# Performance work log

Hardware: AMD Instinct MI355X
Metric: run time of the kernel (lower is better)

Reference implementation:

```python
import jax, jax.numpy as jnp
import numpy as np
from jax import lax

B = 65536

def _conv(x, w, b):
    y = lax.conv_general_dilated(x, w, (1, 1), 'VALID',
                                 dimension_numbers=('NCHW', 'OIHW', 'NCHW'))
    return y + b[None, :, None, None]

def _maxpool2(x):
    return lax.reduce_window(x, -jnp.inf, lax.max, (1, 1, 2, 2), (1, 1, 2, 2), 'VALID')

def _cnot01(s):  # control wire0, target wire1; s: [B,2,2] indexed [b,q0,q1]
    return jnp.stack([s[:, 0, :], s[:, 1, ::-1]], axis=1)

def _cnot10(s):  # control wire1, target wire0
    return jnp.stack([s[:, :, 0], s[:, ::-1, 1]], axis=2)

def _ry(half_angle):  # RY(2*half_angle) as used in circuit (theta/2 = half_angle)
    c, si = jnp.cos(half_angle), jnp.sin(half_angle)
    return jnp.stack([jnp.stack([c, -si]), jnp.stack([si, c])]).astype(jnp.complex64)

def _apply_w0(s, U):
    return jnp.einsum('ij,bjk->bik', U, s)

def _apply_w1(s, U):
    return jnp.einsum('ij,bkj->bki', U, s)

def _quantum(x2, p):
    # x2: [B,2] float32, p: [8] float32. Batched 2-qubit statevector sim.
    x0, x1 = x2[:, 0], x2[:, 1]
    n = x2.shape[0]
    s = jnp.full((n, 2, 2), 0.5 + 0.0j, dtype=jnp.complex64)  # H|0> x H|0>
    # RZ(2*x0) on wire 0: diag(e^{-i x0}, e^{i x0})
    s = s * jnp.exp(1j * jnp.stack([-x0, x0], axis=1).astype(jnp.complex64))[:, :, None]
    # RZ(2*x1) on wire 1
    s = s * jnp.exp(1j * jnp.stack([-x1, x1], axis=1).astype(jnp.complex64))[:, None, :]
    s = _cnot01(s)
    ang = (jnp.pi - x0) * (jnp.pi - x1)  # RZ(2*ang) on wire 1
    s = s * jnp.exp(1j * jnp.stack([-ang, ang], axis=1).astype(jnp.complex64))[:, None, :]
    s = _cnot01(s)
    s = _apply_w0(s, _ry(p[0])); s = _apply_w1(s, _ry(p[1])); s = _cnot01(s)
    s = _apply_w0(s, _ry(p[2])); s = _apply_w1(s, _ry(p[3])); s = _cnot10(s)
    s = _apply_w0(s, _ry(p[4])); s = _apply_w1(s, _ry(p[5])); s = _cnot01(s)
    s = _apply_w0(s, _ry(p[6])); s = _apply_w1(s, _ry(p[7]))
    z = jnp.array([[1.0, -1.0], [-1.0, 1.0]], dtype=jnp.float32)  # Z0 (x) Z1 signs
    prob = (s.real ** 2 + s.imag ** 2)
    return jnp.sum(prob * z[None], axis=(1, 2))  # [B]

def setup_inputs() -> dict:
    key = jax.random.key(0)
    ks = jax.random.split(key, 12)
    d = {}
    d['x'] = jax.random.normal(ks[0], (B, 1, 28, 28), dtype=jnp.float32)
    d['conv1_w'] = jax.random.normal(ks[1], (2, 1, 5, 5), dtype=jnp.float32) * 0.2
    d['conv1_b'] = jax.random.normal(ks[2], (2,), dtype=jnp.float32) * 0.1
    d['conv2_w'] = jax.random.normal(ks[3], (16, 2, 5, 5), dtype=jnp.float32) * 0.14
    d['conv2_b'] = jax.random.normal(ks[4], (16,), dtype=jnp.float32) * 0.1
    d['fc1_w'] = jax.random.normal(ks[5], (64, 256), dtype=jnp.float32) * 0.0625
    d['fc1_b'] = jax.random.normal(ks[6], (64,), dtype=jnp.float32) * 0.05
    d['fc2_w'] = jax.random.normal(ks[7], (2, 64), dtype=jnp.float32) * 0.125
    d['fc2_b'] = jax.random.normal(ks[8], (2,), dtype=jnp.float32) * 0.05
    d['fc3_w'] = jax.random.normal(ks[9], (1, 1), dtype=jnp.float32)
    d['fc3_b'] = jax.random.normal(ks[10], (1,), dtype=jnp.float32) * 0.05
    d['qnn_params'] = jax.random.uniform(ks[11], (8,), dtype=jnp.float32)
    return d

def reference(x, conv1_w, conv1_b, conv2_w, conv2_b, fc1_w, fc1_b,
              fc2_w, fc2_b, fc3_w, fc3_b, qnn_params):
    h = jax.nn.relu(_conv(x, conv1_w, conv1_b))        # [B,2,24,24]
    h = _maxpool2(h)                                    # [B,2,12,12]
    h = jax.nn.relu(_conv(h, conv2_w, conv2_b))        # [B,16,8,8]
    h = _maxpool2(h)                                    # [B,16,4,4]
    # Dropout2d: identity in eval mode
    h = h.reshape(h.shape[0], -1)                       # [B,256]
    h = jax.nn.relu(h @ fc1_w.T + fc1_b)                # [B,64]
    h = h @ fc2_w.T + fc2_b                             # [B,2]
    q = _quantum(h, qnn_params)[:, None]                # [B,1]
    y = q @ fc3_w.T + fc3_b                             # [B,1]
    logits = jnp.concatenate([y, 1.0 - y], axis=-1)     # [B,2]
    return jax.nn.log_softmax(logits, axis=1)
```

## Files before the change

### kernel.cpp

```cpp
#include <hip/hip_runtime.h>
#include <math.h>


typedef float v2f __attribute__((ext_vector_type(2)));
typedef float f32x4 __attribute__((ext_vector_type(4)));
typedef short bf16x8 __attribute__((ext_vector_type(8)));

union B8 { unsigned int u[4]; bf16x8 v; };

static __device__ __forceinline__ v2f vfma2(v2f a, float w, v2f c) {
    return __builtin_elementwise_fma(a, (v2f){w, w}, c);
}
static __device__ __forceinline__ v2f vmax2(v2f a, v2f b) {
    return __builtin_elementwise_max(a, b);
}

#define PK_FMA_W0(acc, w, xp) \
    asm("v_pk_fma_f32 %0, %1, %2, %0 op_sel:[0,0,0] op_sel_hi:[1,0,1]" \
        : "+v"(acc) : "s"(w), "v"(xp))
#define PK_FMA_W1(acc, w, xp) \
    asm("v_pk_fma_f32 %0, %1, %2, %0 op_sel:[0,1,0] op_sel_hi:[1,1,1]" \
        : "+v"(acc) : "s"(w), "v"(xp))

#define MFMA16(a, b, c) __builtin_amdgcn_mfma_f32_16x16x32_bf16(a, b, c, 0, 0, 0)

static __device__ __forceinline__ void pack_hilo(const float* f, bf16x8& bh, bf16x8& bl) {
    B8 H, L;
    #pragma unroll
    for (int jp = 0; jp < 4; ++jp) {
        unsigned int u0 = __float_as_uint(f[2 * jp]);
        unsigned int u1 = __float_as_uint(f[2 * jp + 1]);
        H.u[jp] = (u1 & 0xFFFF0000u) | (u0 >> 16);
        float l0 = f[2 * jp]     - __uint_as_float(u0 & 0xFFFF0000u);
        float l1 = f[2 * jp + 1] - __uint_as_float(u1 & 0xFFFF0000u);
        L.u[jp] = (__float_as_uint(l1) & 0xFFFF0000u) | (__float_as_uint(l0) >> 16);
    }
    bh = H.v; bl = L.v;
}

#define A2_HI 0
#define A2_LO 1024
#define A1_HI 2048
#define A1_LO (2048 + 16384)

#define P1_S 292
#define HB_S 260

__global__ __launch_bounds__(256)
void hqcnn_prep(const float* __restrict__ w2, const float* __restrict__ fw1,
                unsigned short* __restrict__ ws) {
    int t = blockIdx.x * 256 + threadIdx.x;
    if (blockIdx.x == 0) {
        for (int e = threadIdx.x; e < 1024; e += 256) {
            int m = e >> 6, k = e & 63;
            int c = k >> 5, uv = k & 31;
            float val = (uv < 25) ? w2[m * 50 + c * 25 + uv] : 0.f;
            unsigned int u = __float_as_uint(val);
            float lo = val - __uint_as_float(u & 0xFFFF0000u);
            ws[A2_HI + e] = (unsigned short)(u >> 16);
            ws[A2_LO + e] = (unsigned short)(__float_as_uint(lo) >> 16);
        }
    }
    for (int e = t; e < 16384; e += gridDim.x * 256) {
        float val = fw1[e];
        unsigned int u = __float_as_uint(val);
        float lo = val - __uint_as_float(u & 0xFFFF0000u);
        ws[A1_HI + e] = (unsigned short)(u >> 16);
        ws[A1_LO + e] = (unsigned short)(__float_as_uint(lo) >> 16);
    }
}

__global__ __launch_bounds__(256, 6)
void hqcnn_fused(const float* __restrict__ x,
                 const float* __restrict__ w1,
                 const float* __restrict__ b1,
                 const float* __restrict__ b2,
                 const float* __restrict__ fb1,
                 const float* __restrict__ fw2,
                 const float* __restrict__ fb2,
                 const float* __restrict__ fw3,
                 const float* __restrict__ fb3,
                 const float* __restrict__ qp,
                 const unsigned short* __restrict__ ws,
                 float* __restrict__ out)
{
    __shared__ __align__(16) float p1s[8 * P1_S];
    __shared__ __align__(16) float hbs[8 * HB_S];
    __shared__ __align__(16) float zbuf[4 * 32];

    const int t = threadIdx.x;
    const int wv = t >> 6;
    const int lane = t & 63;
    const int n = lane & 15;
    const int q = lane >> 4;
    const long base = (long)blockIdx.x * 8;

    {
        v2f w1p[25];
        #pragma unroll
        for (int k = 0; k < 25; ++k)
            w1p[k] = (v2f){w1[k], w1[25 + k]};
        const v2f bias1 = (v2f){b1[0], b1[1]};

        #pragma unroll
        for (int it = 0; it < 2; ++it) {
            int f = lane + it * 64;
            if (f < 96) {
                int s = f / 48;
                int r = f - s * 48;
                int i = r >> 2, jh = r & 3;
                const float* xrow = x + (base + 2 * wv + s) * 784;
                v2f acc[12];
                #pragma unroll
                for (int qq = 0; qq < 12; ++qq) acc[qq] = (v2f){0.f, 0.f};
                #pragma unroll
                for (int u = 0; u < 6; ++u) {
                    const v2f* xp = (const v2f*)(xrow + (2 * i + u) * 28 + 6 * jh);
                    v2f P[5] = { xp[0], xp[1], xp[2], xp[3], xp[4] };
                    #pragma unroll
                    for (int a = 0; a < 2; ++a) {
                        if (a <= u && (u - a) <= 4) {
                            const int wu = u - a;
                            #pragma unroll
                            for (int v = 0; v < 5; ++v) {
                                #pragma unroll
                                for (int j = 0; j < 6; ++j) {
                                    const int e = j + v;
                                    if (e & 1) { PK_FMA_W1(acc[a * 6 + j], w1p[wu * 5 + v], P[e >> 1]); }
                                    else       { PK_FMA_W0(acc[a * 6 + j], w1p[wu * 5 + v], P[e >> 1]); }
                                }
                            }
                        }
                    }
                }
                #pragma unroll
                for (int m = 0; m < 3; ++m) {
                    v2f mx = vmax2(vmax2(acc[2 * m], acc[2 * m + 1]),
                                   vmax2(acc[6 + 2 * m], acc[7 + 2 * m]));
                    mx = mx + bias1;
                    mx = vmax2(mx, (v2f){0.f, 0.f});
                    int pc = 3 * jh + m;
                    int off = (2 * wv + s) * P1_S + i * 12 + pc;
                    p1s[off] = mx.x;
                    p1s[off + 144] = mx.y;
                }
            }
        }
    }
    asm volatile("s_waitcnt lgkmcnt(0)" ::: "memory");

    {
        const bf16x8* A2h = (const bf16x8*)(ws + A2_HI);
        const bf16x8* A2l = (const bf16x8*)(ws + A2_LO);
        bf16x8 a_h0 = A2h[n * 8 + q],     a_h1 = A2h[n * 8 + 4 + q];
        bf16x8 a_l0 = A2l[n * 8 + q],     a_l1 = A2l[n * 8 + 4 + q];

        int offs[8]; bool vld[8];
        #pragma unroll
        for (int j = 0; j < 8; ++j) {
            int uv = q * 8 + j;
            int u = (uv * 205) >> 10;
            int v = uv - u * 5;
            bool ok = uv < 25;
            offs[j] = ok ? (u * 12 + v) : 0;
            vld[j] = ok;
        }
        f32x4 bias4 = *(const f32x4*)(b2 + q * 4);

        for (int t8 = 0; t8 < 8; ++t8) {
            int smp = 2 * wv + (t8 >> 2);
            int tt = t8 & 3;
            int prow = 2 * tt + (n >> 3);
            int pcol = n & 7;
            f32x4 acc = {0.f, 0.f, 0.f, 0.f};
            #pragma unroll
            for (int c = 0; c < 2; ++c) {
                int pb = smp * P1_S + c * 144 + prow * 12 + pcol;
                float fv[8];
                #pragma unroll
                for (int j = 0; j < 8; ++j) {
                    float xv = p1s[pb + offs[j]];
                    fv[j] = vld[j] ? xv : 0.f;
                }
                bf16x8 bh, bl;
                pack_hilo(fv, bh, bl);
                bf16x8 ah = c ? a_h1 : a_h0;
                bf16x8 al = c ? a_l1 : a_l0;
                acc = MFMA16(ah, bh, acc);
                acc = MFMA16(ah, bl, acc);
                acc = MFMA16(al, bh, acc);
            }
            #pragma unroll
            for (int r = 0; r < 4; ++r) {
                float vmx = acc[r];
                vmx = fmaxf(vmx, __shfl_xor(vmx, 1, 64));
                vmx = fmaxf(vmx, __shfl_xor(vmx, 8, 64));
                float pv = fmaxf(vmx + bias4[r], 0.f);
                if ((n & 1) == 0 && n < 8) {
                    int jc = n >> 1;
                    hbs[smp * HB_S + (q * 4 + r) * 16 + tt * 4 + jc] = pv;
                }
            }
        }
    }
    __syncthreads();

    {
        const bf16x8* A1h = (const bf16x8*)(ws + A1_HI);
        const bf16x8* A1l = (const bf16x8*)(ws + A1_LO);
        const int abase = (wv * 16 + n) * 32 + q;
        f32x4 acc = {0.f, 0.f, 0.f, 0.f};
        #pragma unroll
        for (int kk = 0; kk < 8; ++kk) {
            bf16x8 ah = A1h[abase + kk * 4];
            bf16x8 al = A1l[abase + kk * 4];
            float fv[8];
            if (n < 8) {
                const f32x4* hp = (const f32x4*)(hbs + n * HB_S + kk * 32 + q * 8);
                f32x4 h0 = hp[0], h1 = hp[1];
                fv[0] = h0.x; fv[1] = h0.y; fv[2] = h0.z; fv[3] = h0.w;
                fv[4] = h1.x; fv[5] = h1.y; fv[6] = h1.z; fv[7] = h1.w;
            } else {
                #pragma unroll
                for (int j = 0; j < 8; ++j) fv[j] = 0.f;
            }
            bf16x8 bh, bl;
            pack_hilo(fv, bh, bl);
            acc = MFMA16(ah, bh, acc);
            acc = MFMA16(ah, bl, acc);
            acc = MFMA16(al, bh, acc);
        }
        f32x4 fb4 = *(const f32x4*)(fb1 + wv * 16 + q * 4);
        f32x4 w20 = *(const f32x4*)(fw2 + wv * 16 + q * 4);
        f32x4 w21 = *(const f32x4*)(fw2 + 64 + wv * 16 + q * 4);
        float p0 = 0.f, p1v = 0.f;
        #pragma unroll
        for (int r = 0; r < 4; ++r) {
            float a = fmaxf(acc[r] + fb4[r], 0.f);
            p0  = fmaf(a, w20[r], p0);
            p1v = fmaf(a, w21[r], p1v);
        }
        p0  += __shfl_xor(p0, 16, 64);  p0  += __shfl_xor(p0, 32, 64);
        p1v += __shfl_xor(p1v, 16, 64); p1v += __shfl_xor(p1v, 32, 64);
        if (q == 0) {
            zbuf[wv * 32 + n * 2]     = p0;
            zbuf[wv * 32 + n * 2 + 1] = p1v;
        }
    }
    __syncthreads();

    {
        int s = t & 7;
        float x0 = fb2[0] + zbuf[s * 2]     + zbuf[32 + s * 2]
                          + zbuf[64 + s * 2] + zbuf[96 + s * 2];
        float x1 = fb2[1] + zbuf[s * 2 + 1] + zbuf[32 + s * 2 + 1]
                          + zbuf[64 + s * 2 + 1] + zbuf[96 + s * 2 + 1];

        float sr[4], si[4];
        {
            float th0 = -x0 - x1, th1 = -x0 + x1, th2 = x0 - x1, th3 = x0 + x1;
            sr[0] = 0.5f * __cosf(th0); si[0] = 0.5f * __sinf(th0);
            sr[1] = 0.5f * __cosf(th1); si[1] = 0.5f * __sinf(th1);
            sr[2] = 0.5f * __cosf(th2); si[2] = 0.5f * __sinf(th2);
            sr[3] = 0.5f * __cosf(th3); si[3] = 0.5f * __sinf(th3);
        }
        {
            float tr = sr[2]; sr[2] = sr[3]; sr[3] = tr;
            float ti = si[2]; si[2] = si[3]; si[3] = ti;
            float ang = ((float)M_PI - x0) * ((float)M_PI - x1);
            float ca = __cosf(ang), sa = __sinf(ang);
            float r, im;
            r = sr[0]; im = si[0]; sr[0] = r*ca + im*sa; si[0] = im*ca - r*sa;
            r = sr[2]; im = si[2]; sr[2] = r*ca + im*sa; si[2] = im*ca - r*sa;
            r = sr[1]; im = si[1]; sr[1] = r*ca - im*sa; si[1] = im*ca + r*sa;
            r = sr[3]; im = si[3]; sr[3] = r*ca - im*sa; si[3] = im*ca + r*sa;
            tr = sr[2]; sr[2] = sr[3]; sr[3] = tr;
            ti = si[2]; si[2] = si[3]; si[3] = ti;
        }
        float cp[8], sp[8];
        #pragma unroll
        for (int g = 0; g < 8; ++g) { float qv = qp[g]; cp[g] = __cosf(qv); sp[g] = __sinf(qv); }

        #define QRY0(cc, ss) { \
            float a0r=sr[0], a0i=si[0], a1r=sr[2], a1i=si[2]; \
            sr[0]=cc*a0r-ss*a1r; si[0]=cc*a0i-ss*a1i; \
            sr[2]=ss*a0r+cc*a1r; si[2]=ss*a0i+cc*a1i; \
            float b0r=sr[1], b0i=si[1], b1r=sr[3], b1i=si[3]; \
            sr[1]=cc*b0r-ss*b1r; si[1]=cc*b0i-ss*b1i; \
            sr[3]=ss*b0r+cc*b1r; si[3]=ss*b0i+cc*b1i; }
        #define QRY1(cc, ss) { \
            float a0r=sr[0], a0i=si[0], a1r=sr[1], a1i=si[1]; \
            sr[0]=cc*a0r-ss*a1r; si[0]=cc*a0i-ss*a1i; \
            sr[1]=ss*a0r+cc*a1r; si[1]=ss*a0i+cc*a1i; \
            float b0r=sr[2], b0i=si[2], b1r=sr[3], b1i=si[3]; \
            sr[2]=cc*b0r-ss*b1r; si[2]=cc*b0i-ss*b1i; \
            sr[3]=ss*b0r+cc*b1r; si[3]=ss*b0i+cc*b1i; }
        #define QSWAP(i_, j_) { float tr=sr[i_]; sr[i_]=sr[j_]; sr[j_]=tr; \
                                float ti=si[i_]; si[i_]=si[j_]; si[j_]=ti; }

        QRY0(cp[0], sp[0]);
        QRY1(cp[1], sp[1]);
        QSWAP(2, 3);
        QRY0(cp[2], sp[2]);
        QRY1(cp[3], sp[3]);
        QSWAP(1, 3);
        QRY0(cp[4], sp[4]);
        QRY1(cp[5], sp[5]);
        QSWAP(2, 3);
        QRY0(cp[6], sp[6]);
        QRY1(cp[7], sp[7]);

        float qv = (sr[0]*sr[0] + si[0]*si[0])
                 - (sr[1]*sr[1] + si[1]*si[1])
                 - (sr[2]*sr[2] + si[2]*si[2])
                 + (sr[3]*sr[3] + si[3]*si[3]);
        float y = fmaf(qv, fw3[0], fb3[0]);
        float l0 = y, l1 = 1.0f - y;
        float m = fmaxf(l0, l1);
        float lse = m + __logf(__expf(l0 - m) + __expf(l1 - m));
        if (t < 16) {
            int comp = t >> 3;
            out[(base + s) * 2 + comp] = comp ? (l1 - lse) : (l0 - lse);
        }
        #undef QRY0
        #undef QRY1
        #undef QSWAP
    }
}

extern "C" void kernel_launch(void* const* d_in, const int* in_sizes, int n_in,
                              void* d_out, int out_size, void* d_ws, size_t ws_size,
                              hipStream_t stream) {
    const float* x   = (const float*)d_in[0];
    const float* w1  = (const float*)d_in[1];
    const float* b1  = (const float*)d_in[2];
    const float* w2  = (const float*)d_in[3];
    const float* b2  = (const float*)d_in[4];
    const float* fw1 = (const float*)d_in[5];
    const float* fb1 = (const float*)d_in[6];
    const float* fw2 = (const float*)d_in[7];
    const float* fb2 = (const float*)d_in[8];
    const float* fw3 = (const float*)d_in[9];
    const float* fb3 = (const float*)d_in[10];
    const float* qp  = (const float*)d_in[11];
    float* outp = (float*)d_out;
    unsigned short* wsp = (unsigned short*)d_ws;

    hipLaunchKernelGGL(hqcnn_prep, dim3(64), dim3(256), 0, stream, w2, fw1, wsp);

    int B = in_sizes[0] / 784;
    int nblk = B / 8;
    hipLaunchKernelGGL(hqcnn_fused, dim3(nblk), dim3(256), 0, stream,
                       x, w1, b1, b2, fb1, fw2, fb2, fw3, fb3, qp, wsp, outp);
}
```

Before: 396.9 us.

## Store activations pre-split into bf16 hi/lo pairs and repack conv2 K layout

Intermediate activations in shared memory are now stored as packed bf16 hi/lo words at write time, so the MFMA consumers split them with v_perm instead of re-running the float split per element. The conv2 weight layout is reorganised into three K-chunks of 5-wide rows, so each lane reads five contiguous words, and the old validity masks and offset tables are replaced by a zeroed pad region. A second accumulator splits the dependent MFMA chain. The trade is an extra third MFMA K-chunk in conv2 in return for less ALU work and simpler LDS addressing.

```diff
diff --git a/kernel.cpp b/kernel.cpp
--- a/kernel.cpp
+++ b/kernel.cpp
@@ -5,12 +5,10 @@
 typedef float v2f __attribute__((ext_vector_type(2)));
 typedef float f32x4 __attribute__((ext_vector_type(4)));
 typedef short bf16x8 __attribute__((ext_vector_type(8)));
+typedef unsigned int u32x4 __attribute__((ext_vector_type(4)));
 
 union B8 { unsigned int u[4]; bf16x8 v; };
 
-static __device__ __forceinline__ v2f vfma2(v2f a, float w, v2f c) {
-    return __builtin_elementwise_fma(a, (v2f){w, w}, c);
-}
 static __device__ __forceinline__ v2f vmax2(v2f a, v2f b) {
     return __builtin_elementwise_max(a, b);
 }
@@ -24,26 +22,21 @@
 
 #define MFMA16(a, b, c) __builtin_amdgcn_mfma_f32_16x16x32_bf16(a, b, c, 0, 0, 0)
 
-static __device__ __forceinline__ void pack_hilo(const float* f, bf16x8& bh, bf16x8& bl) {
-    B8 H, L;
-    #pragma unroll
-    for (int jp = 0; jp < 4; ++jp) {
-        unsigned int u0 = __float_as_uint(f[2 * jp]);
-        unsigned int u1 = __float_as_uint(f[2 * jp + 1]);
-        H.u[jp] = (u1 & 0xFFFF0000u) | (u0 >> 16);
-        float l0 = f[2 * jp]     - __uint_as_float(u0 & 0xFFFF0000u);
-        float l1 = f[2 * jp + 1] - __uint_as_float(u1 & 0xFFFF0000u);
-        L.u[jp] = (__float_as_uint(l1) & 0xFFFF0000u) | (__float_as_uint(l0) >> 16);
-    }
-    bh = H.v; bl = L.v;
+#define SEL_HI 0x07060302u
+#define SEL_LO 0x05040100u
+
+static __device__ __forceinline__ unsigned int pack1(float v) {
+    unsigned int hi = __float_as_uint(v) & 0xFFFF0000u;
+    float lo = v - __uint_as_float(hi);
+    return hi | (__float_as_uint(lo) >> 16);
 }
 
 #define A2_HI 0
-#define A2_LO 1024
-#define A1_HI 2048
-#define A1_LO (2048 + 16384)
-
-#define P1_S 292
+#define A2_LO 1536
+#define A1_HI 3072
+#define A1_LO (3072 + 16384)
+
+#define P1_S 296
 #define HB_S 260
 
 __global__ __launch_bounds__(256)
@@ -51,13 +44,17 @@
                 unsigned short* __restrict__ ws) {
     int t = blockIdx.x * 256 + threadIdx.x;
     if (blockIdx.x == 0) {
-        for (int e = threadIdx.x; e < 1024; e += 256) {
-            int m = e >> 6, k = e & 63;
-            int c = k >> 5, uv = k & 31;
-            float val = (uv < 25) ? w2[m * 50 + c * 25 + uv] : 0.f;
-            unsigned int u = __float_as_uint(val);
-            float lo = val - __uint_as_float(u & 0xFFFF0000u);
-            ws[A2_HI + e] = (unsigned short)(u >> 16);
+        for (int e = threadIdx.x; e < 1536; e += 256) {
+            int cc = e >> 9, r = e & 511;
+            int m = r >> 5, kl = r & 31;
+            int q = kl >> 3, j = kl & 7;
+            int row = cc * 4 + q;
+            int ch = (row >= 5) ? 1 : 0;
+            int u = row - 5 * ch;
+            float val = (row < 10 && j < 5) ? w2[m * 50 + ch * 25 + u * 5 + j] : 0.f;
+            unsigned int uu = __float_as_uint(val);
+            float lo = val - __uint_as_float(uu & 0xFFFF0000u);
+            ws[A2_HI + e] = (unsigned short)(uu >> 16);
             ws[A2_LO + e] = (unsigned short)(__float_as_uint(lo) >> 16);
         }
     }
@@ -84,8 +81,8 @@
                  const unsigned short* __restrict__ ws,
                  float* __restrict__ out)
 {
-    __shared__ __align__(16) float p1s[8 * P1_S];
-    __shared__ __align__(16) float hbs[8 * HB_S];
+    __shared__ __align__(16) unsigned int p1u[8 * P1_S];
+    __shared__ __align__(16) unsigned int hbu[8 * HB_S];
     __shared__ __align__(16) float zbuf[4 * 32];
 
     const int t = threadIdx.x;
@@ -94,6 +91,9 @@
     const int n = lane & 15;
     const int q = lane >> 4;
     const long base = (long)blockIdx.x * 8;
+
+    if (lane < 16)
+        p1u[(2 * wv + (lane >> 3)) * P1_S + 288 + (lane & 7)] = 0u;
 
     {
         v2f w1p[25];
@@ -141,8 +141,8 @@
                     mx = vmax2(mx, (v2f){0.f, 0.f});
                     int pc = 3 * jh + m;
                     int off = (2 * wv + s) * P1_S + i * 12 + pc;
-                    p1s[off] = mx.x;
-                    p1s[off + 144] = mx.y;
+                    p1u[off] = pack1(mx.x);
+                    p1u[off + 144] = pack1(mx.y);
                 }
             }
         }
@@ -152,18 +152,19 @@
     {
         const bf16x8* A2h = (const bf16x8*)(ws + A2_HI);
         const bf16x8* A2l = (const bf16x8*)(ws + A2_LO);
-        bf16x8 a_h0 = A2h[n * 8 + q],     a_h1 = A2h[n * 8 + 4 + q];
-        bf16x8 a_l0 = A2l[n * 8 + q],     a_l1 = A2l[n * 8 + 4 + q];
-
-        int offs[8]; bool vld[8];
-        #pragma unroll
-        for (int j = 0; j < 8; ++j) {
-            int uv = q * 8 + j;
-            int u = (uv * 205) >> 10;
-            int v = uv - u * 5;
-            bool ok = uv < 25;
-            offs[j] = ok ? (u * 12 + v) : 0;
-            vld[j] = ok;
+        bf16x8 a_h[3], a_l[3];
+        #pragma unroll
+        for (int cc = 0; cc < 3; ++cc) {
+            a_h[cc] = A2h[cc * 64 + n * 4 + q];
+            a_l[cc] = A2l[cc * 64 + n * 4 + q];
+        }
+        int chu[3];
+        #pragma unroll
+        for (int cc = 0; cc < 3; ++cc) {
+            int row = cc * 4 + q;
+            int ch = (row >= 5) ? 1 : 0;
+            int u = row - 5 * ch;
+            chu[cc] = (row < 10) ? (ch * 144 + u * 12) : -1;
         }
         f32x4 bias4 = *(const f32x4*)(b2 + q * 4);
 
@@ -172,24 +173,29 @@
             int tt = t8 & 3;
             int prow = 2 * tt + (n >> 3);
             int pcol = n & 7;
+            int pbase = smp * P1_S + prow * 12 + pcol;
+            int zaddr = smp * P1_S + 288;
             f32x4 acc = {0.f, 0.f, 0.f, 0.f};
+            f32x4 acc2 = {0.f, 0.f, 0.f, 0.f};
             #pragma unroll
-            for (int c = 0; c < 2; ++c) {
-                int pb = smp * P1_S + c * 144 + prow * 12 + pcol;
-                float fv[8];
-                #pragma unroll
-                for (int j = 0; j < 8; ++j) {
-                    float xv = p1s[pb + offs[j]];
-                    fv[j] = vld[j] ? xv : 0.f;
-                }
-                bf16x8 bh, bl;
-                pack_hilo(fv, bh, bl);
-                bf16x8 ah = c ? a_h1 : a_h0;
-                bf16x8 al = c ? a_l1 : a_l0;
-                acc = MFMA16(ah, bh, acc);
-                acc = MFMA16(ah, bl, acc);
-                acc = MFMA16(al, bh, acc);
+            for (int cc = 0; cc < 3; ++cc) {
+                int a = (chu[cc] >= 0) ? (pbase + chu[cc]) : zaddr;
+                unsigned int e0 = p1u[a],     e1 = p1u[a + 1], e2 = p1u[a + 2],
+                             e3 = p1u[a + 3], e4 = p1u[a + 4];
+                B8 BH, BL;
+                BH.u[0] = __builtin_amdgcn_perm(e1, e0, SEL_HI);
+                BH.u[1] = __builtin_amdgcn_perm(e3, e2, SEL_HI);
+                BH.u[2] = e4 >> 16;
+                BH.u[3] = 0u;
+                BL.u[0] = __builtin_amdgcn_perm(e1, e0, SEL_LO);
+                BL.u[1] = __builtin_amdgcn_perm(e3, e2, SEL_LO);
+                BL.u[2] = e4 & 0xFFFFu;
+                BL.u[3] = 0u;
+                acc  = MFMA16(a_h[cc], BH.v, acc);
+                acc2 = MFMA16(a_h[cc], BL.v, acc2);
+                acc  = MFMA16(a_l[cc], BH.v, acc);
             }
+            acc = acc + acc2;
             #pragma unroll
             for (int r = 0; r < 4; ++r) {
                 float vmx = acc[r];
@@ -198,7 +204,7 @@
                 float pv = fmaxf(vmx + bias4[r], 0.f);
                 if ((n & 1) == 0 && n < 8) {
                     int jc = n >> 1;
-                    hbs[smp * HB_S + (q * 4 + r) * 16 + tt * 4 + jc] = pv;
+                    hbu[smp * HB_S + (q * 4 + r) * 16 + tt * 4 + jc] = pack1(pv);
                 }
             }
         }
@@ -210,26 +216,32 @@
         const bf16x8* A1l = (const bf16x8*)(ws + A1_LO);
         const int abase = (wv * 16 + n) * 32 + q;
         f32x4 acc = {0.f, 0.f, 0.f, 0.f};
+        f32x4 acc2 = {0.f, 0.f, 0.f, 0.f};
         #pragma unroll
         for (int kk = 0; kk < 8; ++kk) {
             bf16x8 ah = A1h[abase + kk * 4];
             bf16x8 al = A1l[abase + kk * 4];
-            float fv[8];
+            B8 BH, BL;
             if (n < 8) {
-                const f32x4* hp = (const f32x4*)(hbs + n * HB_S + kk * 32 + q * 8);
-                f32x4 h0 = hp[0], h1 = hp[1];
-                fv[0] = h0.x; fv[1] = h0.y; fv[2] = h0.z; fv[3] = h0.w;
-                fv[4] = h1.x; fv[5] = h1.y; fv[6] = h1.z; fv[7] = h1.w;
+                const u32x4* hp = (const u32x4*)(hbu + n * HB_S + kk * 32 + q * 8);
+                u32x4 d0 = hp[0], d1 = hp[1];
+                BH.u[0] = __builtin_amdgcn_perm(d0.y, d0.x, SEL_HI);
+                BH.u[1] = __builtin_amdgcn_perm(d0.w, d0.z, SEL_HI);
+                BH.u[2] = __builtin_amdgcn_perm(d1.y, d1.x, SEL_HI);
+                BH.u[3] = __builtin_amdgcn_perm(d1.w, d1.z, SEL_HI);
+                BL.u[0] = __builtin_amdgcn_perm(d0.y, d0.x, SEL_LO);
+                BL.u[1] = __builtin_amdgcn_perm(d0.w, d0.z, SEL_LO);
+                BL.u[2] = __builtin_amdgcn_perm(d1.y, d1.x, SEL_LO);
+                BL.u[3] = __builtin_amdgcn_perm(d1.w, d1.z, SEL_LO);
             } else {
-                #pragma unroll
-                for (int j = 0; j < 8; ++j) fv[j] = 0.f;
+                BH.u[0] = BH.u[1] = BH.u[2] = BH.u[3] = 0u;
+                BL.u[0] = BL.u[1] = BL.u[2] = BL.u[3] = 0u;
             }
-            bf16x8 bh, bl;
-            pack_hilo(fv, bh, bl);
-            acc = MFMA16(ah, bh, acc);
-            acc = MFMA16(ah, bl, acc);
-            acc = MFMA16(al, bh, acc);
-        }
+            acc  = MFMA16(ah, BH.v, acc);
+            acc2 = MFMA16(ah, BL.v, acc2);
+            acc  = MFMA16(al, BH.v, acc);
+        }
+        acc = acc + acc2;
         f32x4 fb4 = *(const f32x4*)(fb1 + wv * 16 + q * 4);
         f32x4 w20 = *(const f32x4*)(fw2 + wv * 16 + q * 4);
         f32x4 w21 = *(const f32x4*)(fw2 + 64 + wv * 16 + q * 4);
```

Result: no change. 402.1 us (+1.3%).
